# Kernel optimization log

Hardware: AMD Instinct MI355X
Metric: run time of the kernel (lower is better)

The kernel has to match this reference:

```python
import jax, jax.numpy as jnp
import numpy as np

N_NODES = 20000
N_EDGES = 320000
N_GRAPHS = 32
IN_CH = 5
HID = 64
HEADS = 4
DH = HID // HEADS  # 16
LAYERS = 8
EPS = 1e-5
SLOPE = 0.2


def setup_inputs() -> dict:
    key = jax.random.key(0)
    ks = jax.random.split(key, 32)
    inp = {}
    inp['x1'] = jax.random.normal(ks[0], (N_NODES, IN_CH), dtype=jnp.float32)
    inp['x2'] = jax.random.normal(ks[1], (N_NODES, IN_CH), dtype=jnp.float32)
    inp['edge_index1'] = jax.random.randint(ks[2], (2, N_EDGES), 0, N_NODES, dtype=jnp.int32)
    inp['edge_index2'] = jax.random.randint(ks[3], (2, N_EDGES), 0, N_NODES, dtype=jnp.int32)
    inp['batch1'] = jnp.sort(jax.random.randint(ks[4], (N_NODES,), 0, N_GRAPHS, dtype=jnp.int32))
    inp['batch2'] = jnp.sort(jax.random.randint(ks[5], (N_NODES,), 0, N_GRAPHS, dtype=jnp.int32))
    # node_lin
    inp['Wn'] = jax.random.normal(ks[6], (IN_CH, HID), dtype=jnp.float32) / np.sqrt(IN_CH)
    inp['bnode'] = jnp.zeros((HID,), dtype=jnp.float32)
    # GATv2 layers (stacked over LAYERS)
    s = 1.0 / np.sqrt(HID)
    inp['Wl'] = jax.random.normal(ks[7], (LAYERS, HID, HID), dtype=jnp.float32) * s
    inp['bl'] = jnp.zeros((LAYERS, HID), dtype=jnp.float32)
    inp['Wr'] = jax.random.normal(ks[8], (LAYERS, HID, HID), dtype=jnp.float32) * s
    inp['br'] = jnp.zeros((LAYERS, HID), dtype=jnp.float32)
    inp['att'] = jax.random.normal(ks[9], (LAYERS, HEADS, DH), dtype=jnp.float32) / np.sqrt(DH)
    inp['cbias'] = jnp.zeros((LAYERS, HID), dtype=jnp.float32)
    # batch norms
    inp['gamma'] = jnp.ones((LAYERS, HID), dtype=jnp.float32)
    inp['beta'] = jnp.zeros((LAYERS, HID), dtype=jnp.float32)
    # fc head
    inp['f1w'] = jax.random.normal(ks[10], (2 * HID, 256), dtype=jnp.float32) / np.sqrt(2 * HID)
    inp['f1b'] = jnp.zeros((256,), dtype=jnp.float32)
    inp['f2w'] = jax.random.normal(ks[11], (256, 128), dtype=jnp.float32) / np.sqrt(256)
    inp['f2b'] = jnp.zeros((128,), dtype=jnp.float32)
    inp['f3w'] = jax.random.normal(ks[12], (128, 1), dtype=jnp.float32) / np.sqrt(128)
    inp['f3b'] = jnp.zeros((1,), dtype=jnp.float32)
    return inp


def _gatv2_layer(x, src, dst, Wl, bl, Wr, br, att, bias):
    # x: [N, HID]; src/dst: [E'] (self loops included)
    N = x.shape[0]
    xl = (x @ Wl + bl).reshape(N, HEADS, DH)  # source transform
    xr = (x @ Wr + br).reshape(N, HEADS, DH)  # target transform
    e = jax.nn.leaky_relu(xl[src] + xr[dst], SLOPE)          # [E, H, DH]
    score = jnp.einsum('ehd,hd->eh', e, att)                  # [E, H]
    smax = jax.ops.segment_max(score, dst, num_segments=N)    # [N, H]
    ex = jnp.exp(score - smax[dst])
    denom = jax.ops.segment_sum(ex, dst, num_segments=N)
    alpha = ex / denom[dst]                                   # [E, H]
    msg = alpha[:, :, None] * xl[src]                         # [E, H, DH]
    out = jax.ops.segment_sum(msg, dst, num_segments=N)       # [N, H, DH]
    return out.reshape(N, HID) + bias


def _forward_once(x, edge_index, batch, Wn, bnode, Wl, bl, Wr, br, att, cbias, gamma, beta):
    N = x.shape[0]
    loop = jnp.arange(N, dtype=edge_index.dtype)
    src = jnp.concatenate([edge_index[0], loop])  # add_self_loops=True
    dst = jnp.concatenate([edge_index[1], loop])
    h = x @ Wn + bnode
    for l in range(LAYERS):
        g = _gatv2_layer(h, src, dst, Wl[l], bl[l], Wr[l], br[l], att[l], cbias[l])
        mu = g.mean(axis=0)
        var = g.var(axis=0)
        g = (g - mu) / jnp.sqrt(var + EPS) * gamma[l] + beta[l]
        h = h + jax.nn.elu(g)
    # global_mean_pool
    sums = jax.ops.segment_sum(h, batch, num_segments=N_GRAPHS)
    cnt = jax.ops.segment_sum(jnp.ones((N,), dtype=h.dtype), batch, num_segments=N_GRAPHS)
    return sums / jnp.maximum(cnt, 1.0)[:, None]


def reference(x1, edge_index1, batch1, x2, edge_index2, batch2, Wn, bnode, Wl, bl, Wr, br, att, cbias, gamma, beta, f1w, f1b, f2w, f2b, f3w, f3b):
    o1 = _forward_once(x1, edge_index1, batch1, Wn, bnode, Wl, bl, Wr, br, att, cbias, gamma, beta)
    o2 = _forward_once(x2, edge_index2, batch2, Wn, bnode, Wl, bl, Wr, br, att, cbias, gamma, beta)
    c = jnp.concatenate([o1, o2], axis=1)           # [G, 128]
    h = jax.nn.relu(c @ f1w + f1b)                   # dropout = identity (eval)
    h = jax.nn.relu(h @ f2w + f2b)
    return h @ f3w + f3b                             # [G, 1]
```

## Files before the change

kernel.cpp:

```cpp
#include <hip/hip_runtime.h>
#include <hip/hip_bf16.h>
#include <hip/hip_fp16.h>

#define N_NODES 20000
#define HID 64
#define EPS 1e-5f

typedef _Float16 h2 __attribute__((ext_vector_type(2)));

struct GP {
    const int* ei;
    const int* batch;
    const float* x;
    int* deg;
    int* cursor;
    int* csr;
    float* h;
    __half* xlh;
    __half* xrh;
    float* gb;
    float* stats;
    float* osum;
};


__global__ void k_csr_init(GP a, GP b, int n, int two) {
    int t = blockIdx.x * blockDim.x + threadIdx.x;
    if (t < n) {
        a.deg[t] = 1;
        if (two) b.deg[t] = 1;
    }
}

__global__ void k_count(GP a, GP b, int Ea, int Eb, int two) {
    int t = blockIdx.x * blockDim.x + threadIdx.x;
    if (t < Ea) atomicAdd(&a.deg[a.ei[Ea + t]], 1);
    if (two && t < Eb) atomicAdd(&b.deg[b.ei[Eb + t]], 1);
}

#define SCAN_T 1024
#define SCAN_C 20
__global__ __launch_bounds__(1024) void k_scan(GP a, GP b, int n, int totA, int totB) {
    GP g = blockIdx.x ? b : a;
    int total = blockIdx.x ? totB : totA;
    __shared__ int sd[SCAN_T];
    int t = threadIdx.x;
    int base = t * SCAN_C;
    int loc[SCAN_C];
    int s = 0;
#pragma unroll
    for (int i = 0; i < SCAN_C; ++i) {
        int idx = base + i;
        loc[i] = (idx < n) ? g.deg[idx] : 0;
        s += loc[i];
    }
    sd[t] = s;
    __syncthreads();
    for (int off = 1; off < SCAN_T; off <<= 1) {
        int v = (t >= off) ? sd[t - off] : 0;
        __syncthreads();
        sd[t] += v;
        __syncthreads();
    }
    int run = sd[t] - s;
#pragma unroll
    for (int i = 0; i < SCAN_C; ++i) {
        int idx = base + i;
        if (idx < n) { g.deg[idx] = run; g.cursor[idx] = run; run += loc[i]; }
    }
    if (t == 0) g.deg[n] = total;
}

__global__ void k_scatter(GP a, GP b, int Ea, int Eb, int n, int two) {
    int t = blockIdx.x * blockDim.x + threadIdx.x;
    if (t < Ea) {
        int s = a.ei[t], d = a.ei[Ea + t];
        a.csr[atomicAdd(&a.cursor[d], 1)] = s * 128;
    } else if (t < Ea + n) {
        int nn = t - Ea;
        a.csr[atomicAdd(&a.cursor[nn], 1)] = nn * 128;
    }
    if (two) {
        if (t < Eb) {
            int s = b.ei[t], d = b.ei[Eb + t];
            b.csr[atomicAdd(&b.cursor[d], 1)] = s * 128;
        } else if (t < Eb + n) {
            int nn = t - Eb;
            b.csr[atomicAdd(&b.cursor[nn], 1)] = nn * 128;
        }
    }
}


__global__ void k_nodelin(GP a, GP b, int nPer, const float* __restrict__ Wn,
                          const float* __restrict__ bn, int n) {
    int bid = blockIdx.x;
    GP g = a;
    if (bid >= nPer) { g = b; bid -= nPer; }
    int idx = bid * 256 + threadIdx.x;
    if (idx >= n * HID) return;
    int node = idx >> 6, c = idx & 63;
    float acc = bn[c];
#pragma unroll
    for (int k = 0; k < 5; ++k) acc += g.x[node * 5 + k] * Wn[k * HID + c];
    g.h[idx] = acc;
}


__global__ __launch_bounds__(256) void k_lin2(GP ga, GP gbp, int nPer, int n,
        const float* __restrict__ Wl, const float* __restrict__ bl,
        const float* __restrict__ Wr, const float* __restrict__ br,
        const float* __restrict__ gamma, const float* __restrict__ beta, int layer) {
    __shared__ float wls[4096], wrs[4096];
    __shared__ float hs[2048];
    int bid = blockIdx.x;
    GP g = ga;
    if (bid >= nPer) { g = gbp; bid -= nPer; }
    {
        const float4* wl4 = (const float4*)Wl;
        const float4* wr4 = (const float4*)Wr;
        float4* l4 = (float4*)wls;
        float4* r4 = (float4*)wrs;
        for (int i = threadIdx.x; i < 1024; i += 256) { l4[i] = wl4[i]; r4[i] = wr4[i]; }
    }
    int c = threadIdx.x & 63;
    int wid = threadIdx.x >> 6;
    float blv = bl[c], brv = br[c];
    float mu = 0.f, inv = 1.f, gam = 1.f, bet = 0.f;
    if (layer > 0) {
        const float* st = g.stats + (layer - 1) * 128;
        float invn = 1.0f / (float)n;
        mu = st[c] * invn;
        float var = st[64 + c] * invn - mu * mu;
        inv = rsqrtf(fmaxf(var, 0.f) + EPS);
        gam = gamma[c]; bet = beta[c];
    }
    __syncthreads();
    float* hw = &hs[wid * 512];
    const float4* hw4 = (const float4*)hw;
    for (int base = bid * 32; base < n; base += nPer * 32) {
        int nb = base + wid * 8;
        size_t off0 = (size_t)nb * 64 + c;
        float hv[8];
        if (layer > 0) {
#pragma unroll
            for (int j = 0; j < 8; ++j) {
                float gv = g.gb[off0 + j * 64];
                float ov = g.h[off0 + j * 64];
                float v = (gv - mu) * inv * gam + bet;
                v = v > 0.f ? v : expm1f(v);
                hv[j] = ov + v;
                g.h[off0 + j * 64] = hv[j];
            }
        } else {
#pragma unroll
            for (int j = 0; j < 8; ++j) hv[j] = g.h[off0 + j * 64];
        }
#pragma unroll
        for (int j = 0; j < 8; ++j) hw[j * 64 + c] = hv[j];
        float accl[8], accr[8];
#pragma unroll
        for (int j = 0; j < 8; ++j) { accl[j] = blv; accr[j] = brv; }
        for (int k4 = 0; k4 < 16; ++k4) {
            float4 hq[8];
#pragma unroll
            for (int j = 0; j < 8; ++j) hq[j] = hw4[j * 16 + k4];
#pragma unroll
            for (int kk = 0; kk < 4; ++kk) {
                float wl = wls[(k4 * 4 + kk) * 64 + c];
                float wr = wrs[(k4 * 4 + kk) * 64 + c];
#pragma unroll
                for (int j = 0; j < 8; ++j) {
                    float hx = (&hq[j].x)[kk];
                    accl[j] = fmaf(hx, wl, accl[j]);
                    accr[j] = fmaf(hx, wr, accr[j]);
                }
            }
        }
#pragma unroll
        for (int j = 0; j < 8; ++j) {
            g.xlh[off0 + j * 64] = __float2half(accl[j]);
            g.xrh[off0 + j * 64] = __float2half(accr[j]);
        }
    }
}


__device__ __forceinline__ float red8(float p) {
    p += __int_as_float(__builtin_amdgcn_update_dpp(0, __float_as_int(p), 0xB1, 0xF, 0xF, true));
    p += __int_as_float(__builtin_amdgcn_update_dpp(0, __float_as_int(p), 0x4E, 0xF, 0xF, true));
    p += __int_as_float(__builtin_amdgcn_update_dpp(0, __float_as_int(p), 0x141, 0xF, 0xF, true));
    return p;
}

__global__ __launch_bounds__(1024) void k_attn(GP ga, GP gbp, int nPer,
        const float* __restrict__ att, const float* __restrict__ cbias, int layer, int n) {
    int bid = blockIdx.x;
    GP g = (bid & 1) ? gbp : ga;
    bid >>= 1;
    int lane = threadIdx.x & 63;
    int wid = threadIdx.x >> 6;
    int hh = lane >> 5;
    int cl = lane & 31;
    int gw = bid * 16 + wid;
    int nw = nPer * 16;
    const float LOG2E = 1.44269504f;
    float a0 = att[2 * cl] * LOG2E;
    float a1 = att[2 * cl + 1] * LOG2E;
    float cb0 = cbias[2 * cl], cb1 = cbias[2 * cl + 1];
    const h2 slope = {(_Float16)0.2f, (_Float16)0.2f};
    const int* __restrict__ rowptr = g.deg;
    const int* __restrict__ csr = g.csr;
    const char* xlb = (const char*)g.xlh + (size_t)cl * 4;
    const char* xrb = (const char*)g.xrh + (size_t)cl * 4;
    float* __restrict__ gbuf = g.gb;
    float* st = g.stats + layer * 128;
    float bs0 = 0.f, bs1 = 0.f, bq0 = 0.f, bq1 = 0.f;
    for (int node = gw; node < n; node += nw) {
        int start = rowptr[node], end = rowptr[node + 1];
        h2 xrv = *(const h2*)(xrb + (size_t)node * 128);
        float sself;
        {
            h2 xs = *(const h2*)(xlb + (size_t)node * 128);
            h2 t = xs + xrv;
            h2 lk = __builtin_elementwise_max(t, t * slope);
            float sp = fmaf((float)lk.x, a0, (float)lk.y * a1);
            sself = red8(sp);
        }
        float lsum = 0.f, acc0 = 0.f, acc1 = 0.f;
        int idx = start;
        for (; idx + 16 <= end; idx += 16) {
            int off[8];
            h2 xv[8];
#pragma unroll
            for (int j = 0; j < 8; ++j) off[j] = csr[idx + 2 * j + hh];
#pragma unroll
            for (int j = 0; j < 8; ++j) xv[j] = *(const h2*)(xlb + off[j]);
#pragma unroll
            for (int j = 0; j < 8; ++j) {
                h2 t = xv[j] + xrv;
                h2 lk = __builtin_elementwise_max(t, t * slope);
                float sp = fmaf((float)lk.x, a0, (float)lk.y * a1);
                float w = exp2f(fminf(red8(sp) - sself, 110.f));
                lsum += w;
                acc0 = fmaf(w, (float)xv[j].x, acc0);
                acc1 = fmaf(w, (float)xv[j].y, acc1);
            }
        }
        for (; idx + 8 <= end; idx += 8) {
            int off[4];
            h2 xv[4];
#pragma unroll
            for (int j = 0; j < 4; ++j) off[j] = csr[idx + 2 * j + hh];
#pragma unroll
            for (int j = 0; j < 4; ++j) xv[j] = *(const h2*)(xlb + off[j]);
#pragma unroll
            for (int j = 0; j < 4; ++j) {
                h2 t = xv[j] + xrv;
                h2 lk = __builtin_elementwise_max(t, t * slope);
                float sp = fmaf((float)lk.x, a0, (float)lk.y * a1);
                float w = exp2f(fminf(red8(sp) - sself, 110.f));
                lsum += w;
                acc0 = fmaf(w, (float)xv[j].x, acc0);
                acc1 = fmaf(w, (float)xv[j].y, acc1);
            }
        }
        for (; idx < end; idx += 2) {
            int e = idx + hh;
            bool valid = e < end;
            int off = csr[valid ? e : end - 1];
            h2 xv = *(const h2*)(xlb + off);
            h2 t = xv + xrv;
            h2 lk = __builtin_elementwise_max(t, t * slope);
            float sp = fmaf((float)lk.x, a0, (float)lk.y * a1);
            float w = exp2f(fminf(red8(sp) - sself, 110.f));
            w = valid ? w : 0.f;
            lsum += w;
            acc0 = fmaf(w, (float)xv.x, acc0);
            acc1 = fmaf(w, (float)xv.y, acc1);
        }
        lsum += __shfl_xor(lsum, 32);
        acc0 += __shfl_xor(acc0, 32);
        acc1 += __shfl_xor(acc1, 32);
        if (hh == 0) {
            float invl = 1.0f / lsum;
            float o0 = acc0 * invl + cb0;
            float o1 = acc1 * invl + cb1;
            float2 o = {o0, o1};
            *(float2*)(gbuf + (size_t)node * 64 + 2 * cl) = o;
            bs0 += o0; bs1 += o1;
            bq0 += o0 * o0; bq1 += o1 * o1;
        }
    }
    __shared__ float2 sred[1024];
    float2 z = {0.f, 0.f};
    float2 v1 = {bs0, bs1};
    sred[threadIdx.x] = (hh == 0) ? v1 : z;
    __syncthreads();
    if (threadIdx.x < 32) {
        float t0 = 0.f, t1 = 0.f;
#pragma unroll
        for (int w = 0; w < 16; ++w) { float2 s = sred[w * 64 + threadIdx.x]; t0 += s.x; t1 += s.y; }
        atomicAdd(&st[2 * threadIdx.x], t0);
        atomicAdd(&st[2 * threadIdx.x + 1], t1);
    }
    __syncthreads();
    float2 v2 = {bq0, bq1};
    sred[threadIdx.x] = (hh == 0) ? v2 : z;
    __syncthreads();
    if (threadIdx.x < 32) {
        float t0 = 0.f, t1 = 0.f;
#pragma unroll
        for (int w = 0; w < 16; ++w) { float2 s = sred[w * 64 + threadIdx.x]; t0 += s.x; t1 += s.y; }
        atomicAdd(&st[64 + 2 * threadIdx.x], t0);
        atomicAdd(&st[64 + 2 * threadIdx.x + 1], t1);
    }
}


__global__ __launch_bounds__(256) void k_pool(GP ga, GP gbp, int nPer,
        const float* __restrict__ gamma, const float* __restrict__ beta, int n) {
    int bid = blockIdx.x;
    GP g = ga;
    if (bid >= nPer) { g = gbp; bid -= nPer; }
    int lane = threadIdx.x & 63, w = threadIdx.x >> 6;
    const float* st = g.stats + 7 * 128;
    float invn = 1.f / (float)n;
    float mu = st[lane] * invn;
    float var = st[64 + lane] * invn - mu * mu;
    float inv = rsqrtf(fmaxf(var, 0.f) + EPS);
    float gam = gamma[lane], bet = beta[lane];
    int chunk = (n + nPer - 1) / nPer;
    int s = bid * chunk;
    int e = min(s + chunk, n);
    float acc = 0.f;
    int cur = -1;
    for (int node = s + w; node < e; node += 4) {
        int bg = g.batch[node];
        size_t off = (size_t)node * 64 + lane;
        float gv = g.gb[off];
        float hv = g.h[off];
        float v = (gv - mu) * inv * gam + bet;
        float hn = hv + (v > 0.f ? v : expm1f(v));
        if (bg != cur) {
            if (cur >= 0) atomicAdd(&g.osum[cur * 64 + lane], acc);
            acc = 0.f; cur = bg;
        }
        acc += hn;
    }
    if (cur >= 0) atomicAdd(&g.osum[cur * 64 + lane], acc);
}


__device__ __forceinline__ int lb(const int* __restrict__ b, int n, int v) {
    int lo = 0, hi = n;
    while (lo < hi) { int mid = (lo + hi) >> 1; if (b[mid] < v) lo = mid + 1; else hi = mid; }
    return lo;
}

__global__ __launch_bounds__(256) void k_fc(const float* __restrict__ o1, const float* __restrict__ o2,
                                            const int* __restrict__ b1, const int* __restrict__ b2,
                                            const float* __restrict__ f1w, const float* __restrict__ f1b,
                                            const float* __restrict__ f2w, const float* __restrict__ f2b,
                                            const float* __restrict__ f3w, const float* __restrict__ f3b,
                                            float* __restrict__ out, int n) {
    int gid = blockIdx.x, t = threadIdx.x;
    __shared__ float cin[128];
    __shared__ float h1[256];
    __shared__ float red[128];
    __shared__ int cnts[2];
    if (t == 0) cnts[0] = lb(b1, n, gid + 1) - lb(b1, n, gid);
    if (t == 1) cnts[1] = lb(b2, n, gid + 1) - lb(b2, n, gid);
    __syncthreads();
    if (t < 64) {
        float c1 = (float)(cnts[0] > 0 ? cnts[0] : 1);
        float c2 = (float)(cnts[1] > 0 ? cnts[1] : 1);
        cin[t] = o1[gid * 64 + t] / c1;
        cin[64 + t] = o2[gid * 64 + t] / c2;
    }
    __syncthreads();
    float a = f1b[t];
#pragma unroll 8
    for (int k = 0; k < 128; ++k) a += cin[k] * f1w[k * 256 + t];
    h1[t] = fmaxf(a, 0.f);
    __syncthreads();
    if (t < 128) {
        float a2 = f2b[t];
#pragma unroll 8
        for (int k = 0; k < 256; ++k) a2 += h1[k] * f2w[k * 128 + t];
        red[t] = fmaxf(a2, 0.f) * f3w[t];
    }
    __syncthreads();
    for (int off = 64; off > 0; off >>= 1) {
        if (t < off) red[t] += red[t + off];
        __syncthreads();
    }
    if (t == 0) out[gid] = red[0] + f3b[0];
}


extern "C" void kernel_launch(void* const* d_in, const int* in_sizes, int n_in,
                              void* d_out, int out_size, void* d_ws, size_t ws_size,
                              hipStream_t stream) {
    const float* x1 = (const float*)d_in[0];
    const float* x2 = (const float*)d_in[1];
    const int* ei1 = (const int*)d_in[2];
    const int* ei2 = (const int*)d_in[3];
    const int* b1 = (const int*)d_in[4];
    const int* b2 = (const int*)d_in[5];
    const float* Wn = (const float*)d_in[6];
    const float* bnode = (const float*)d_in[7];
    const float* Wl = (const float*)d_in[8];
    const float* bl = (const float*)d_in[9];
    const float* Wr = (const float*)d_in[10];
    const float* br = (const float*)d_in[11];
    const float* att = (const float*)d_in[12];
    const float* cbias = (const float*)d_in[13];
    const float* gamma = (const float*)d_in[14];
    const float* beta = (const float*)d_in[15];
    const float* f1w = (const float*)d_in[16];
    const float* f1b = (const float*)d_in[17];
    const float* f2w = (const float*)d_in[18];
    const float* f2b = (const float*)d_in[19];
    const float* f3w = (const float*)d_in[20];
    const float* f3b = (const float*)d_in[21];
    float* out = (float*)d_out;

    const int N = N_NODES;
    const int EA = in_sizes[2] / 2;
    const int EB = in_sizes[3] / 2;
    const size_t INT_PG = 20096 + 20096 + 340096;
    const size_t BIG = (size_t)N * 64;
    const size_t SMALL = 2 * 1024 + 2 * 2048;
    const size_t dualBytes = 2 * INT_PG * 4 + (8 * BIG + SMALL) * 4;
    const int dual = (ws_size >= dualBytes) ? 1 : 0;

    int* ibase = (int*)d_ws;
    int* iA = ibase;
    int* iB = dual ? ibase + INT_PG : ibase;
    float* fbase = (float*)(ibase + (size_t)(dual ? 2 : 1) * INT_PG);
    float* hA = fbase;
    float* xlA = hA + BIG;
    float* xrA = xlA + BIG;
    float* gbA = xrA + BIG;
    float* hB = dual ? gbA + BIG : hA;
    float* xlB = dual ? hB + BIG : xlA;
    float* xrB = dual ? xlB + BIG : xrA;
    float* gbB = dual ? xrB + BIG : gbA;
    float* small = dual ? gbB + BIG : gbA + BIG;
    float* statsA = small;
    float* statsB = small + 1024;
    float* osumA = small + 2048;
    float* osumB = small + 4096;

    GP A, B;
    A.ei = ei1; A.batch = b1; A.x = x1;
    A.deg = iA; A.cursor = iA + 20096; A.csr = iA + 40192;
    A.h = hA; A.xlh = (__half*)xlA; A.xrh = (__half*)xrA;
    A.gb = gbA; A.stats = statsA; A.osum = osumA;
    B.ei = ei2; B.batch = b2; B.x = x2;
    B.deg = iB; B.cursor = iB + 20096; B.csr = iB + 40192;
    B.h = hB; B.xlh = (__half*)xlB; B.xrh = (__half*)xrB;
    B.gb = gbB; B.stats = statsB; B.osum = osumB;

    hipMemsetAsync(small, 0, SMALL * sizeof(float), stream);

    const int LIN2_NB = 320;
    const int ATT_NB = 256;
    const int POOL_NB = 250;

    if (dual) {
        int Emax = EA > EB ? EA : EB;
        k_csr_init<<<(N + 255) / 256, 256, 0, stream>>>(A, B, N, 1);
        k_count<<<(Emax + 255) / 256, 256, 0, stream>>>(A, B, EA, EB, 1);
        k_scan<<<2, 1024, 0, stream>>>(A, B, N, EA + N, EB + N);
        k_scatter<<<(Emax + N + 255) / 256, 256, 0, stream>>>(A, B, EA, EB, N, 1);
        k_nodelin<<<2 * ((N * 64) / 256), 256, 0, stream>>>(A, B, (N * 64) / 256, Wn, bnode, N);
        for (int l = 0; l < 8; ++l) {
            const float* gm = l ? gamma + (l - 1) * 64 : gamma;
            const float* bt = l ? beta + (l - 1) * 64 : beta;
            k_lin2<<<2 * LIN2_NB, 256, 0, stream>>>(A, B, LIN2_NB, N, Wl + l * 4096, bl + l * 64,
                                                    Wr + l * 4096, br + l * 64, gm, bt, l);
            k_attn<<<2 * ATT_NB, 1024, 0, stream>>>(A, B, ATT_NB, att + l * 64, cbias + l * 64, l, N);
        }
        k_pool<<<2 * POOL_NB, 256, 0, stream>>>(A, B, POOL_NB, gamma + 7 * 64, beta + 7 * 64, N);
    } else {
        for (int gi = 0; gi < 2; ++gi) {
            GP G = gi ? B : A;
            int E = gi ? EB : EA;
            k_csr_init<<<(N + 255) / 256, 256, 0, stream>>>(G, G, N, 0);
            k_count<<<(E + 255) / 256, 256, 0, stream>>>(G, G, E, E, 0);
            k_scan<<<1, 1024, 0, stream>>>(G, G, N, E + N, E + N);
            k_scatter<<<(E + N + 255) / 256, 256, 0, stream>>>(G, G, E, E, N, 0);
            k_nodelin<<<(N * 64) / 256, 256, 0, stream>>>(G, G, (N * 64) / 256, Wn, bnode, N);
            for (int l = 0; l < 8; ++l) {
                const float* gm = l ? gamma + (l - 1) * 64 : gamma;
                const float* bt = l ? beta + (l - 1) * 64 : beta;
                k_lin2<<<LIN2_NB, 256, 0, stream>>>(G, G, LIN2_NB, N, Wl + l * 4096, bl + l * 64,
                                                    Wr + l * 4096, br + l * 64, gm, bt, l);
                k_attn<<<2 * ATT_NB, 1024, 0, stream>>>(G, G, ATT_NB, att + l * 64, cbias + l * 64, l, N);
            }
            k_pool<<<POOL_NB, 256, 0, stream>>>(G, G, POOL_NB, gamma + 7 * 64, beta + 7 * 64, N);
        }
    }
    k_fc<<<32, 256, 0, stream>>>(osumA, osumB, b1, b2, f1w, f1b, f2w, f2b, f3w, f3b, out, N);
}
```

Before: 660.0 us.

## Use fp16 packed dot2 for linear projections with prepacked weights

Adds a one-time kernel that converts Wl/Wr to packed half2 pairs along K, and rewrites k_lin2 to stage h in fp16 shared memory and accumulate with fdot2. The grid grows to 625 blocks per graph so each block handles exactly one 32-node tile, which removes the grid-stride loop. This halves shared-memory and weight traffic and halves the FMA count. The cost is reduced precision in the inputs to the projection, and the kernel now assumes N is exactly 625*32 with no bounds check.

```diff
diff --git a/kernel.cpp b/kernel.cpp
--- a/kernel.cpp
+++ b/kernel.cpp
@@ -1,12 +1,15 @@
 #include <hip/hip_runtime.h>
 #include <hip/hip_bf16.h>
 #include <hip/hip_fp16.h>
+#include <stdint.h>
 
 #define N_NODES 20000
 #define HID 64
 #define EPS 1e-5f
 
 typedef _Float16 h2 __attribute__((ext_vector_type(2)));
+
+__device__ __forceinline__ h2 u2h(uint32_t u) { union { uint32_t u; h2 h; } v; v.u = u; return v.h; }
 
 struct GP {
     const int* ei;
@@ -92,6 +95,26 @@
 }
 
 
+__global__ void k_wcvt(const float* __restrict__ Wl, const float* __restrict__ Wr,
+                       uint32_t* __restrict__ wpk) {
+    int t = blockIdx.x * 256 + threadIdx.x;
+    if (t >= 16384) return;
+    int l = t >> 11, r = t & 2047;
+    int k2 = r >> 6, c = r & 63;
+    const float* wl = Wl + l * 4096;
+    const float* wr = Wr + l * 4096;
+    h2 a, b;
+    a.x = (_Float16)wl[(2 * k2) * 64 + c];
+    a.y = (_Float16)wl[(2 * k2 + 1) * 64 + c];
+    b.x = (_Float16)wr[(2 * k2) * 64 + c];
+    b.y = (_Float16)wr[(2 * k2 + 1) * 64 + c];
+    union { h2 h; uint32_t u; } ua, ub;
+    ua.h = a; ub.h = b;
+    wpk[l * 4096 + r] = ua.u;
+    wpk[l * 4096 + 2048 + r] = ub.u;
+}
+
+
 __global__ void k_nodelin(GP a, GP b, int nPer, const float* __restrict__ Wn,
                           const float* __restrict__ bn, int n) {
     int bid = blockIdx.x;
@@ -108,20 +131,18 @@
 
 
 __global__ __launch_bounds__(256) void k_lin2(GP ga, GP gbp, int nPer, int n,
-        const float* __restrict__ Wl, const float* __restrict__ bl,
-        const float* __restrict__ Wr, const float* __restrict__ br,
+        const uint32_t* __restrict__ wl2g, const float* __restrict__ bl,
+        const uint32_t* __restrict__ wr2g, const float* __restrict__ br,
         const float* __restrict__ gamma, const float* __restrict__ beta, int layer) {
-    __shared__ float wls[4096], wrs[4096];
-    __shared__ float hs[2048];
+    __shared__ uint32_t wl2[2048], wr2[2048];
+    __shared__ _Float16 hs16[2048];
     int bid = blockIdx.x;
     GP g = ga;
     if (bid >= nPer) { g = gbp; bid -= nPer; }
     {
-        const float4* wl4 = (const float4*)Wl;
-        const float4* wr4 = (const float4*)Wr;
-        float4* l4 = (float4*)wls;
-        float4* r4 = (float4*)wrs;
-        for (int i = threadIdx.x; i < 1024; i += 256) { l4[i] = wl4[i]; r4[i] = wr4[i]; }
+        uint4* dl = (uint4*)wl2; const uint4* sl = (const uint4*)wl2g;
+        uint4* dr = (uint4*)wr2; const uint4* sr = (const uint4*)wr2g;
+        for (int i = threadIdx.x; i < 512; i += 256) { dl[i] = sl[i]; dr[i] = sr[i]; }
     }
     int c = threadIdx.x & 63;
     int wid = threadIdx.x >> 6;
@@ -135,53 +156,51 @@
         inv = rsqrtf(fmaxf(var, 0.f) + EPS);
         gam = gamma[c]; bet = beta[c];
     }
-    __syncthreads();
-    float* hw = &hs[wid * 512];
-    const float4* hw4 = (const float4*)hw;
-    for (int base = bid * 32; base < n; base += nPer * 32) {
-        int nb = base + wid * 8;
-        size_t off0 = (size_t)nb * 64 + c;
-        float hv[8];
-        if (layer > 0) {
+    int nb = bid * 32 + wid * 8;
+    size_t off0 = (size_t)nb * 64 + c;
+    float hv[8];
+    if (layer > 0) {
+#pragma unroll
+        for (int j = 0; j < 8; ++j) {
+            float gv = g.gb[off0 + j * 64];
+            float ov = g.h[off0 + j * 64];
+            float v = (gv - mu) * inv * gam + bet;
+            v = v > 0.f ? v : expm1f(v);
+            hv[j] = ov + v;
+            g.h[off0 + j * 64] = hv[j];
+        }
+    } else {
+#pragma unroll
+        for (int j = 0; j < 8; ++j) hv[j] = g.h[off0 + j * 64];
+    }
+    _Float16* hw16 = &hs16[wid * 512];
+#pragma unroll
+    for (int j = 0; j < 8; ++j) hw16[j * 64 + c] = (_Float16)hv[j];
+    __syncthreads();
+    const uint32_t* hw2 = (const uint32_t*)hw16;
+    float accl[8], accr[8];
+#pragma unroll
+    for (int j = 0; j < 8; ++j) { accl[j] = blv; accr[j] = brv; }
+    for (int k8 = 0; k8 < 8; ++k8) {
+        uint4 hq[8];
+#pragma unroll
+        for (int j = 0; j < 8; ++j) hq[j] = *(const uint4*)&hw2[j * 32 + k8 * 4];
+#pragma unroll
+        for (int p = 0; p < 4; ++p) {
+            h2 wlv = u2h(wl2[(k8 * 4 + p) * 64 + c]);
+            h2 wrv = u2h(wr2[(k8 * 4 + p) * 64 + c]);
 #pragma unroll
             for (int j = 0; j < 8; ++j) {
-                float gv = g.gb[off0 + j * 64];
-                float ov = g.h[off0 + j * 64];
-                float v = (gv - mu) * inv * gam + bet;
-                v = v > 0.f ? v : expm1f(v);
-                hv[j] = ov + v;
-                g.h[off0 + j * 64] = hv[j];
+                h2 hp = u2h((&hq[j].x)[p]);
+                accl[j] = __builtin_amdgcn_fdot2(hp, wlv, accl[j], false);
+                accr[j] = __builtin_amdgcn_fdot2(hp, wrv, accr[j], false);
             }
-        } else {
-#pragma unroll
-            for (int j = 0; j < 8; ++j) hv[j] = g.h[off0 + j * 64];
-        }
-#pragma unroll
-        for (int j = 0; j < 8; ++j) hw[j * 64 + c] = hv[j];
-        float accl[8], accr[8];
-#pragma unroll
-        for (int j = 0; j < 8; ++j) { accl[j] = blv; accr[j] = brv; }
-        for (int k4 = 0; k4 < 16; ++k4) {
-            float4 hq[8];
-#pragma unroll
-            for (int j = 0; j < 8; ++j) hq[j] = hw4[j * 16 + k4];
-#pragma unroll
-            for (int kk = 0; kk < 4; ++kk) {
-                float wl = wls[(k4 * 4 + kk) * 64 + c];
-                float wr = wrs[(k4 * 4 + kk) * 64 + c];
-#pragma unroll
-                for (int j = 0; j < 8; ++j) {
-                    float hx = (&hq[j].x)[kk];
-                    accl[j] = fmaf(hx, wl, accl[j]);
-                    accr[j] = fmaf(hx, wr, accr[j]);
-                }
-            }
-        }
-#pragma unroll
-        for (int j = 0; j < 8; ++j) {
-            g.xlh[off0 + j * 64] = __float2half(accl[j]);
-            g.xrh[off0 + j * 64] = __float2half(accr[j]);
-        }
+        }
+    }
+#pragma unroll
+    for (int j = 0; j < 8; ++j) {
+        g.xlh[off0 + j * 64] = __float2half(accl[j]);
+        g.xrh[off0 + j * 64] = __float2half(accr[j]);
     }
 }
 
@@ -432,7 +451,8 @@
     const size_t INT_PG = 20096 + 20096 + 340096;
     const size_t BIG = (size_t)N * 64;
     const size_t SMALL = 2 * 1024 + 2 * 2048;
-    const size_t dualBytes = 2 * INT_PG * 4 + (8 * BIG + SMALL) * 4;
+    const size_t WPK = 32768;
+    const size_t dualBytes = 2 * INT_PG * 4 + (8 * BIG + SMALL + WPK) * 4;
     const int dual = (ws_size >= dualBytes) ? 1 : 0;
 
     int* ibase = (int*)d_ws;
@@ -452,6 +472,7 @@
     float* statsB = small + 1024;
     float* osumA = small + 2048;
     float* osumB = small + 4096;
+    uint32_t* wpk = (uint32_t*)(small + SMALL);
 
     GP A, B;
     A.ei = ei1; A.batch = b1; A.x = x1;
@@ -465,7 +486,7 @@
 
     hipMemsetAsync(small, 0, SMALL * sizeof(float), stream);
 
-    const int LIN2_NB = 320;
+    const int LIN2_NB = 625;
     const int ATT_NB = 256;
     const int POOL_NB = 250;
 
@@ -475,12 +496,14 @@
         k_count<<<(Emax + 255) / 256, 256, 0, stream>>>(A, B, EA, EB, 1);
         k_scan<<<2, 1024, 0, stream>>>(A, B, N, EA + N, EB + N);
         k_scatter<<<(Emax + N + 255) / 256, 256, 0, stream>>>(A, B, EA, EB, N, 1);
+        k_wcvt<<<64, 256, 0, stream>>>(Wl, Wr, wpk);
         k_nodelin<<<2 * ((N * 64) / 256), 256, 0, stream>>>(A, B, (N * 64) / 256, Wn, bnode, N);
         for (int l = 0; l < 8; ++l) {
             const float* gm = l ? gamma + (l - 1) * 64 : gamma;
             const float* bt = l ? beta + (l - 1) * 64 : beta;
-            k_lin2<<<2 * LIN2_NB, 256, 0, stream>>>(A, B, LIN2_NB, N, Wl + l * 4096, bl + l * 64,
-                                                    Wr + l * 4096, br + l * 64, gm, bt, l);
+            k_lin2<<<2 * LIN2_NB, 256, 0, stream>>>(A, B, LIN2_NB, N,
+                                                    wpk + l * 4096, bl + l * 64,
+                                                    wpk + l * 4096 + 2048, br + l * 64, gm, bt, l);
             k_attn<<<2 * ATT_NB, 1024, 0, stream>>>(A, B, ATT_NB, att + l * 64, cbias + l * 64, l, N);
         }
         k_pool<<<2 * POOL_NB, 256, 0, stream>>>(A, B, POOL_NB, gamma + 7 * 64, beta + 7 * 64, N);
@@ -492,12 +515,14 @@
             k_count<<<(E + 255) / 256, 256, 0, stream>>>(G, G, E, E, 0);
             k_scan<<<1, 1024, 0, stream>>>(G, G, N, E + N, E + N);
             k_scatter<<<(E + N + 255) / 256, 256, 0, stream>>>(G, G, E, E, N, 0);
+            if (gi == 0) k_wcvt<<<64, 256, 0, stream>>>(Wl, Wr, wpk);
             k_nodelin<<<(N * 64) / 256, 256, 0, stream>>>(G, G, (N * 64) / 256, Wn, bnode, N);
             for (int l = 0; l < 8; ++l) {
                 const float* gm = l ? gamma + (l - 1) * 64 : gamma;
                 const float* bt = l ? beta + (l - 1) * 64 : beta;
-                k_lin2<<<LIN2_NB, 256, 0, stream>>>(G, G, LIN2_NB, N, Wl + l * 4096, bl + l * 64,
-                                                    Wr + l * 4096, br + l * 64, gm, bt, l);
+                k_lin2<<<LIN2_NB, 256, 0, stream>>>(G, G, LIN2_NB, N,
+                                                    wpk + l * 4096, bl + l * 64,
+                                                    wpk + l * 4096 + 2048, br + l * 64, gm, bt, l);
                 k_attn<<<2 * ATT_NB, 1024, 0, stream>>>(G, G, ATT_NB, att + l * 64, cbias + l * 64, l, N);
             }
             k_pool<<<POOL_NB, 256, 0, stream>>>(G, G, POOL_NB, gamma + 7 * 64, beta + 7 * 64, N);
```

Measured after the change: 634.4 us. 3.9% less time.
